# Kernel tuning notes

Measured on AMD Instinct MI355X. Metric: run time of the kernel, lower is better.

Reference implementation:

```python
import jax, jax.numpy as jnp
import numpy as np

B, C, H, W = 32, 512, 32, 32
INNER = C // 8


def setup_inputs() -> dict:
    key = jax.random.key(0)
    k_x, k_f, k_g, k_h = jax.random.split(key, 4)
    x = jax.random.normal(k_x, (B, C, H, W), dtype=jnp.float32)
    # 1x1 Conv1d weights (bias=False) are plain [out, in] matrices.
    s_in = 1.0 / np.sqrt(C)
    Wf = jax.random.uniform(k_f, (INNER, C), dtype=jnp.float32, minval=-s_in, maxval=s_in)
    Wg = jax.random.uniform(k_g, (INNER, C), dtype=jnp.float32, minval=-s_in, maxval=s_in)
    Wh = jax.random.uniform(k_h, (C, C), dtype=jnp.float32, minval=-s_in, maxval=s_in)
    return {"x": x, "Wf": Wf, "Wg": Wg, "Wh": Wh}


def reference(x, Wf, Wg, Wh):
    b, c = x.shape[0], x.shape[1]
    xf = x.reshape(b, c, -1)                       # [B, C, N]
    f = jnp.einsum('ic,bcn->bin', Wf, xf)          # [B, inner, N]
    g = jnp.einsum('ic,bcn->bin', Wg, xf)          # [B, inner, N]
    h = jnp.einsum('oc,bcn->bon', Wh, xf)          # [B, C, N]
    sim = jnp.einsum('bin,bim->bnm', f, g)         # f^T g -> [B, N, N]
    beta = jax.nn.softmax(sim, axis=1)             # softmax over the f-index axis (dim=1)
    o = jnp.einsum('bcn,bnm->bcm', h, beta)        # [B, C, N]
    return o
```

## Files before the change

kernel.cpp:

```cpp
#include <hip/hip_runtime.h>
#include <stdint.h>

#define CDIM 512
#define NPIX 1024
#define IDIM 64

#define WS_BATCH (65536 + 65536 + 524288)
#define XT_OFF   ((size_t)32 * WS_BATCH)
#define XT_ELEMS ((size_t)32 * 1024 * 512)
#define WH_OFF   (XT_OFF + XT_ELEMS)
#define P_OFF    XT_OFF
#define P_ELEMS  ((size_t)32 * 1024 * 1024)
#define LP_OFF   (P_OFF + P_ELEMS)

typedef __bf16 bf16x8 __attribute__((ext_vector_type(8)));
typedef _Float16 f16x8 __attribute__((ext_vector_type(8)));
typedef float f32x4 __attribute__((ext_vector_type(4)));

__device__ __forceinline__ unsigned short f2bf(float f) {
    union { float f; uint32_t u; } v; v.f = f;
    uint32_t u = v.u;
    u += 0x7fffu + ((u >> 16) & 1u);
    return (unsigned short)(u >> 16);
}

__device__ __forceinline__ f32x4 mfma_bf(bf16x8 a, bf16x8 b, f32x4 c) {
    return __builtin_amdgcn_mfma_f32_16x16x32_bf16(a, b, c, 0, 0, 0);
}
__device__ __forceinline__ f32x4 mfma_h(f16x8 a, f16x8 b, f32x4 c) {
    return __builtin_amdgcn_mfma_f32_16x16x32_f16(a, b, c, 0, 0, 0);
}
__device__ __forceinline__ void gld_lds16(const void* g, void* l) {
    __builtin_amdgcn_global_load_lds(
        (const __attribute__((address_space(1))) unsigned int*)g,
        (__attribute__((address_space(3))) unsigned int*)l,
        16, 0, 0);
}
__device__ __forceinline__ void barrier_mem() {
    asm volatile("" ::: "memory");
    __builtin_amdgcn_s_barrier();
    asm volatile("" ::: "memory");
}
__device__ __forceinline__ int swz(int by) { return by ^ (((by >> 7) & 3) << 4); }

__global__ __launch_bounds__(256) void wcvt(
    const float* __restrict__ Wf, const float* __restrict__ Wg,
    const float* __restrict__ Wh, _Float16* __restrict__ wh)
{
    int e = (blockIdx.x * 256 + threadIdx.x) * 4;
    int r = e >> 9, k = e & 511;
    const float* src;
    if (r < 64)       src = Wf + (size_t)r * 512 + k;
    else if (r < 128) src = Wg + (size_t)(r - 64) * 512 + k;
    else              src = Wh + (size_t)(r - 128) * 512 + k;
    float4 v = *(const float4*)src;
    _Float16 h4[4] = {(_Float16)v.x, (_Float16)v.y, (_Float16)v.z, (_Float16)v.w};
    *(ushort4*)(wh + e) = *(ushort4*)h4;
}

__global__ __launch_bounds__(256) void xcvt(
    const float* __restrict__ x, _Float16* __restrict__ xT)
{
    __shared__ _Float16 tile[64][72];
    const int b = blockIdx.z, c0 = blockIdx.y * 64, n0 = blockIdx.x * 64;
    const int t = threadIdx.x;
    const float* xb = x + ((size_t)b * CDIM + c0) * NPIX + n0;
    #pragma unroll
    for (int p = 0; p < 4; ++p) {
        int ci = p * 16 + (t >> 4);
        int nj = (t & 15) * 4;
        float4 v = *(const float4*)(xb + (size_t)ci * NPIX + nj);
        tile[nj + 0][ci] = (_Float16)v.x;
        tile[nj + 1][ci] = (_Float16)v.y;
        tile[nj + 2][ci] = (_Float16)v.z;
        tile[nj + 3][ci] = (_Float16)v.w;
    }
    __syncthreads();
    _Float16* dst = xT + ((size_t)b * NPIX + n0) * CDIM + c0;
    #pragma unroll
    for (int p = 0; p < 2; ++p) {
        int n  = p * 32 + (t >> 3);
        int cc = (t & 7) * 8;
        ushort4 a  = *(ushort4*)&tile[n][cc];
        ushort4 bq = *(ushort4*)&tile[n][cc + 4];
        *(ushort4*)(dst + (size_t)n * CDIM + cc)     = a;
        *(ushort4*)(dst + (size_t)n * CDIM + cc + 4) = bq;
    }
}

__global__ __launch_bounds__(256, 4) void fgh_mfma(
    const _Float16* __restrict__ wh, const _Float16* __restrict__ xT,
    unsigned short* __restrict__ ws)
{
    const int orig = blockIdx.x;
    const int work = (orig & 7) * 160 + (orig >> 3);
    const int b    = work / 40;
    const int tile = work % 40;
    const int tr = tile >> 3, tn = tile & 7;

    const int t = threadIdx.x, lane = t & 63, w = t >> 6;
    const int lr = lane & 15, lg = lane >> 4;
    const int wr = w >> 1, wc = w & 1;

    __shared__ _Float16 Abuf[2][128 * 32];
    __shared__ _Float16 Bbuf[2][128 * 32];

    const _Float16* Ag = wh + (size_t)(tr * 128) * CDIM;
    const _Float16* Bg = xT + ((size_t)b * NPIX + tn * 128) * CDIM;

    int offA[4], offB[4];
    #pragma unroll
    for (int mf = 0; mf < 4; ++mf)
        offA[mf] = swz((wr * 64 + mf * 16 + lr) * 64 + lg * 16);
    #pragma unroll
    for (int nf = 0; nf < 4; ++nf)
        offB[nf] = swz((wc * 64 + nf * 16 + lr) * 64 + lg * 16);

    f32x4 acc[4][4];
    #pragma unroll
    for (int i = 0; i < 4; ++i)
        #pragma unroll
        for (int j = 0; j < 4; ++j) acc[i][j] = (f32x4){0.f, 0.f, 0.f, 0.f};

    auto stage = [&](int buf, int k0) {
        #pragma unroll
        for (int p = 0; p < 2; ++p) {
            int q = p * 256 + t;
            gld_lds16(Ag + (size_t)(q >> 2) * CDIM + k0 + ((q & 3) ^ ((q >> 3) & 3)) * 8,
                      (char*)&Abuf[buf][0] + q * 16);
        }
        #pragma unroll
        for (int p = 0; p < 2; ++p) {
            int q = p * 256 + t;
            gld_lds16(Bg + (size_t)(q >> 2) * CDIM + k0 + ((q & 3) ^ ((q >> 3) & 3)) * 8,
                      (char*)&Bbuf[buf][0] + q * 16);
        }
    };

    stage(0, 0);
    stage(1, 32);

    #pragma unroll 1
    for (int ks = 0; ks < 16; ++ks) {
        const int cur = ks & 1;
        if (ks < 15) asm volatile("s_waitcnt vmcnt(4)" ::: "memory");
        else         asm volatile("s_waitcnt vmcnt(0)" ::: "memory");
        barrier_mem();

        const char* Ab = (const char*)&Abuf[cur][0];
        const char* Bb = (const char*)&Bbuf[cur][0];
        f16x8 af[4];
        #pragma unroll
        for (int mf = 0; mf < 4; ++mf)
            af[mf] = *(const f16x8*)(Ab + offA[mf]);
        #pragma unroll
        for (int nf = 0; nf < 4; ++nf) {
            f16x8 bv = *(const f16x8*)(Bb + offB[nf]);
            #pragma unroll
            for (int mf = 0; mf < 4; ++mf)
                acc[mf][nf] = mfma_h(af[mf], bv, acc[mf][nf]);
        }

        barrier_mem();
        if (ks + 2 < 16) stage(cur, (ks + 2) * 32);
    }

    unsigned short* base = ws + (size_t)b * WS_BATCH;
    const int nbase = tn * 128 + wc * 64;
    if (tr == 0) {
        unsigned short* dst = base + (wr ? 65536 : 0);
        #pragma unroll
        for (int mf = 0; mf < 4; ++mf) {
            const int i0 = mf * 16 + lg * 4;
            #pragma unroll
            for (int nf = 0; nf < 4; ++nf) {
                int n = nbase + nf * 16 + lr;
                ushort4 v;
                v.x = f2bf(acc[mf][nf][0]); v.y = f2bf(acc[mf][nf][1]);
                v.z = f2bf(acc[mf][nf][2]); v.w = f2bf(acc[mf][nf][3]);
                *(ushort4*)(dst + (size_t)n * 64 + i0) = v;
            }
        }
    } else {
        unsigned short* hd = base + 131072;
        const int cbase = (tr - 1) * 128 + wr * 64;
        #pragma unroll
        for (int mf = 0; mf < 4; ++mf)
            #pragma unroll
            for (int nf = 0; nf < 4; ++nf) {
                int n = nbase + nf * 16 + lr;
                #pragma unroll
                for (int j = 0; j < 4; ++j) {
                    int c = cbase + mf * 16 + lg * 4 + j;
                    hd[(size_t)c * NPIX + n] = f2bf(acc[mf][nf][j]);
                }
            }
    }
}

__global__ __launch_bounds__(256, 3) void attn_sm(
    const unsigned short* __restrict__ ws, unsigned short* __restrict__ P,
    float* __restrict__ Lp)
{
    const int orig = blockIdx.x;
    const int work = (orig & 7) * 256 + (orig >> 3);
    const int b    = work >> 6;
    const int tile = work & 63;
    const int mt = tile >> 2, nt = tile & 3;
    const int m0 = mt * 64, n0 = nt * 256;

    const int t = threadIdx.x, lane = t & 63, w = t >> 6;
    const int lr = lane & 15, lg = lane >> 4;

    const unsigned short* fT = ws + (size_t)b * WS_BATCH;
    const unsigned short* gT = fT + 65536;

    __shared__ unsigned short Ab[2][64 * 32];
    __shared__ unsigned short Bb[2][256 * 32];
    __shared__ float red[4][64];
    __shared__ unsigned short rp[4][16][72];

    #pragma unroll
    for (int kc = 0; kc < 2; ++kc) {
        {
            int q = t;
            gld_lds16(gT + (size_t)(m0 + (q >> 2)) * 64 + kc * 32 + ((q & 3) ^ ((q >> 3) & 3)) * 8,
                      (char*)&Ab[kc][0] + q * 16);
        }
        #pragma unroll
        for (int p = 0; p < 4; ++p) {
            int q = p * 256 + t;
            gld_lds16(fT + (size_t)(n0 + (q >> 2)) * 64 + kc * 32 + ((q & 3) ^ ((q >> 3) & 3)) * 8,
                      (char*)&Bb[kc][0] + q * 16);
        }
    }
    __syncthreads();

    int offA[4], offB[4];
    #pragma unroll
    for (int mf = 0; mf < 4; ++mf)
        offA[mf] = swz((mf * 16 + lr) * 64 + lg * 16);
    #pragma unroll
    for (int nf = 0; nf < 4; ++nf)
        offB[nf] = swz((w * 64 + nf * 16 + lr) * 64 + lg * 16);

    f32x4 acc[4][4];
    #pragma unroll
    for (int i = 0; i < 4; ++i)
        #pragma unroll
        for (int j = 0; j < 4; ++j) acc[i][j] = (f32x4){0.f, 0.f, 0.f, 0.f};

    #pragma unroll
    for (int kc = 0; kc < 2; ++kc) {
        const char* Abc = (const char*)&Ab[kc][0];
        const char* Bbc = (const char*)&Bb[kc][0];
        bf16x8 af[4];
        #pragma unroll
        for (int mf = 0; mf < 4; ++mf)
            af[mf] = *(const bf16x8*)(Abc + offA[mf]);
        #pragma unroll
        for (int nf = 0; nf < 4; ++nf) {
            bf16x8 bv = *(const bf16x8*)(Bbc + offB[nf]);
            #pragma unroll
            for (int mf = 0; mf < 4; ++mf)
                acc[mf][nf] = mfma_bf(af[mf], bv, acc[mf][nf]);
        }
    }

    #pragma unroll
    for (int mf = 0; mf < 4; ++mf) {
        #pragma unroll
        for (int j = 0; j < 4; ++j) {
            float s = 0.f;
            #pragma unroll
            for (int nf = 0; nf < 4; ++nf) {
                float e = __expf(acc[mf][nf][j]);
                acc[mf][nf][j] = e;
                s += e;
            }
            s += __shfl_xor(s, 1);
            s += __shfl_xor(s, 2);
            s += __shfl_xor(s, 4);
            s += __shfl_xor(s, 8);
            if (lr == 0) red[w][mf * 16 + lg * 4 + j] = s;
        }
    }
    __syncthreads();
    if (t < 64) {
        float s = red[0][t] + red[1][t] + red[2][t] + red[3][t];
        Lp[(size_t)nt * 32768 + (size_t)b * 1024 + m0 + t] = s;
    }

    unsigned short* Pb = P + (size_t)b * NPIX * NPIX;
    #pragma unroll
    for (int mf = 0; mf < 4; ++mf) {
        #pragma unroll
        for (int nf = 0; nf < 4; ++nf)
            #pragma unroll
            for (int j = 0; j < 4; ++j)
                rp[w][lg * 4 + j][nf * 16 + lr] = f2bf(acc[mf][nf][j]);
        #pragma unroll
        for (int ii = 0; ii < 2; ++ii) {
            int row = ii * 8 + (lane >> 3);
            int ch  = lane & 7;
            ushort4 v0 = *(ushort4*)&rp[w][row][ch * 8];
            ushort4 v1 = *(ushort4*)&rp[w][row][ch * 8 + 4];
            unsigned short* dst = Pb + (size_t)(m0 + mf * 16 + row) * NPIX
                                     + n0 + w * 64 + ch * 8;
            *(ushort4*)(dst)     = v0;
            *(ushort4*)(dst + 4) = v1;
        }
    }
}

__global__ __launch_bounds__(256, 4) void attn_pv(
    const unsigned short* __restrict__ P, const unsigned short* __restrict__ ws,
    const float* __restrict__ Lp, float* __restrict__ out)
{
    const int orig = blockIdx.x;
    const int work = (orig & 7) * 128 + (orig >> 3);
    const int b    = work >> 5;
    const int tile = work & 31;
    const int m0   = (tile >> 2) * 128;
    const int c0   = (tile & 3) * 128;

    const int t = threadIdx.x, lane = t & 63, w = t >> 6;
    const int lr = lane & 15, lg = lane >> 4;
    const int wr = w >> 1, wc = w & 1;

    __shared__ unsigned short Abuf[2][128 * 32];
    __shared__ unsigned short Bbuf[2][128 * 32];

    const unsigned short* Ag = P + ((size_t)b * NPIX + m0) * NPIX;
    const unsigned short* Bg = ws + (size_t)b * WS_BATCH + 131072 + (size_t)c0 * NPIX;

    int offA[4], offB[4];
    #pragma unroll
    for (int mf = 0; mf < 4; ++mf)
        offA[mf] = swz((wr * 64 + mf * 16 + lr) * 64 + lg * 16);
    #pragma unroll
    for (int nf = 0; nf < 4; ++nf)
        offB[nf] = swz((wc * 64 + nf * 16 + lr) * 64 + lg * 16);

    f32x4 acc[4][4];
    #pragma unroll
    for (int i = 0; i < 4; ++i)
        #pragma unroll
        for (int j = 0; j < 4; ++j) acc[i][j] = (f32x4){0.f, 0.f, 0.f, 0.f};

    auto stage = [&](int buf, int k0) {
        #pragma unroll
        for (int p = 0; p < 2; ++p) {
            int q = p * 256 + t;
            gld_lds16(Ag + (size_t)(q >> 2) * NPIX + k0 + ((q & 3) ^ ((q >> 3) & 3)) * 8,
                      (char*)&Abuf[buf][0] + q * 16);
        }
        #pragma unroll
        for (int p = 0; p < 2; ++p) {
            int q = p * 256 + t;
            gld_lds16(Bg + (size_t)(q >> 2) * NPIX + k0 + ((q & 3) ^ ((q >> 3) & 3)) * 8,
                      (char*)&Bbuf[buf][0] + q * 16);
        }
    };

    stage(0, 0);
    stage(1, 32);

    #pragma unroll 1
    for (int ks = 0; ks < 32; ++ks) {
        const int cur = ks & 1;
        if (ks < 31) asm volatile("s_waitcnt vmcnt(4)" ::: "memory");
        else         asm volatile("s_waitcnt vmcnt(0)" ::: "memory");
        barrier_mem();

        const char* Ab = (const char*)&Abuf[cur][0];
        const char* Bb = (const char*)&Bbuf[cur][0];
        bf16x8 af[4];
        #pragma unroll
        for (int mf = 0; mf < 4; ++mf)
            af[mf] = *(const bf16x8*)(Ab + offA[mf]);
        #pragma unroll
        for (int nf = 0; nf < 4; ++nf) {
            bf16x8 bv = *(const bf16x8*)(Bb + offB[nf]);
            #pragma unroll
            for (int mf = 0; mf < 4; ++mf)
                acc[mf][nf] = mfma_bf(af[mf], bv, acc[mf][nf]);
        }

        barrier_mem();
        if (ks + 2 < 32) stage(cur, (ks + 2) * 32);
    }

    #pragma unroll
    for (int mf = 0; mf < 4; ++mf) {
        const size_t mi = (size_t)b * 1024 + m0 + wr * 64 + mf * 16 + lg * 4;
        f32x4 L = *(const f32x4*)&Lp[mi]
                + *(const f32x4*)&Lp[32768 + mi]
                + *(const f32x4*)&Lp[65536 + mi]
                + *(const f32x4*)&Lp[98304 + mi];
        f32x4 rinv;
        #pragma unroll
        for (int j = 0; j < 4; ++j) rinv[j] = 1.0f / L[j];
        #pragma unroll
        for (int nf = 0; nf < 4; ++nf) {
            f32x4 o = acc[mf][nf] * rinv;
            int c = c0 + wc * 64 + nf * 16 + lr;
            int m = m0 + wr * 64 + mf * 16 + lg * 4;
            *(f32x4*)(out + ((size_t)b * CDIM + c) * NPIX + m) = o;
        }
    }
}

extern "C" void kernel_launch(void* const* d_in, const int* in_sizes, int n_in,
                              void* d_out, int out_size, void* d_ws, size_t ws_size,
                              hipStream_t stream) {
    const float* x  = (const float*)d_in[0];
    const float* Wf = (const float*)d_in[1];
    const float* Wg = (const float*)d_in[2];
    const float* Wh = (const float*)d_in[3];
    unsigned short* ws = (unsigned short*)d_ws;
    _Float16* xT = (_Float16*)(ws + XT_OFF);
    _Float16* wh = (_Float16*)(ws + WH_OFF);
    unsigned short* P = ws + P_OFF;
    float* Lp = (float*)(ws + LP_OFF);
    float* out = (float*)d_out;

    wcvt<<<320, 256, 0, stream>>>(Wf, Wg, Wh, wh);
    xcvt<<<dim3(16, 8, 32), 256, 0, stream>>>(x, xT);
    fgh_mfma<<<1280, 256, 0, stream>>>(wh, xT, ws);
    attn_sm<<<2048, 256, 0, stream>>>(ws, P, Lp);
    attn_pv<<<1024, 256, 0, stream>>>(P, ws, Lp, out);
}
```

Before: 132.2 us.

## Enlarge attn_pv tiles to 256x256 with 8 waves and interleaved staged prefetch

Reworks the P·V kernel to compute 256x256 output tiles per 512-thread block with a 64-wide K step, using 128KB of LDS and an XOR-swizzled layout. Global-to-LDS loads are split into halves and interleaved between MFMA groups, and s_setprio is raised around the MFMA bursts. The goal is more reuse per byte loaded and better overlap of loads with math. The trade-off is only 256 blocks on a GPU with many CUs, lower occupancy, and heavy LDS and register use.

```diff
diff --git a/kernel.cpp b/kernel.cpp
--- a/kernel.cpp
+++ b/kernel.cpp
@@ -313,87 +313,112 @@
     }
 }
 
-__global__ __launch_bounds__(256, 4) void attn_pv(
+__global__ __launch_bounds__(512, 2) void attn_pv(
     const unsigned short* __restrict__ P, const unsigned short* __restrict__ ws,
     const float* __restrict__ Lp, float* __restrict__ out)
 {
     const int orig = blockIdx.x;
-    const int work = (orig & 7) * 128 + (orig >> 3);
-    const int b    = work >> 5;
-    const int tile = work & 31;
-    const int m0   = (tile >> 2) * 128;
-    const int c0   = (tile & 3) * 128;
+    const int work = (orig & 7) * 32 + (orig >> 3);
+    const int b    = work >> 3;
+    const int tile = work & 7;
+    const int m0   = (tile >> 1) * 256;
+    const int c0   = (tile & 1) * 256;
 
     const int t = threadIdx.x, lane = t & 63, w = t >> 6;
     const int lr = lane & 15, lg = lane >> 4;
-    const int wr = w >> 1, wc = w & 1;
-
-    __shared__ unsigned short Abuf[2][128 * 32];
-    __shared__ unsigned short Bbuf[2][128 * 32];
+    const int wr = w >> 2, wc = w & 3;
+
+    __shared__ __align__(16) char smem[131072];
 
     const unsigned short* Ag = P + ((size_t)b * NPIX + m0) * NPIX;
     const unsigned short* Bg = ws + (size_t)b * WS_BATCH + 131072 + (size_t)c0 * NPIX;
 
-    int offA[4], offB[4];
-    #pragma unroll
-    for (int mf = 0; mf < 4; ++mf)
-        offA[mf] = swz((wr * 64 + mf * 16 + lr) * 64 + lg * 16);
-    #pragma unroll
-    for (int nf = 0; nf < 4; ++nf)
-        offB[nf] = swz((wc * 64 + nf * 16 + lr) * 64 + lg * 16);
-
-    f32x4 acc[4][4];
-    #pragma unroll
-    for (int i = 0; i < 4; ++i)
+    const int sk0 = ((lg) ^ (lr & 7)) * 16;
+    const int sk1 = ((4 + lg) ^ (lr & 7)) * 16;
+    const int rAbase = (wr * 128 + lr) * 128;
+    const int rBbase = (wc * 64 + lr) * 128;
+
+    f32x4 acc[8][4];
+    #pragma unroll
+    for (int i = 0; i < 8; ++i)
         #pragma unroll
         for (int j = 0; j < 4; ++j) acc[i][j] = (f32x4){0.f, 0.f, 0.f, 0.f};
 
-    auto stage = [&](int buf, int k0) {
-        #pragma unroll
-        for (int p = 0; p < 2; ++p) {
-            int q = p * 256 + t;
-            gld_lds16(Ag + (size_t)(q >> 2) * NPIX + k0 + ((q & 3) ^ ((q >> 3) & 3)) * 8,
-                      (char*)&Abuf[buf][0] + q * 16);
-        }
-        #pragma unroll
-        for (int p = 0; p < 2; ++p) {
-            int q = p * 256 + t;
-            gld_lds16(Bg + (size_t)(q >> 2) * NPIX + k0 + ((q & 3) ^ ((q >> 3) & 3)) * 8,
-                      (char*)&Bbuf[buf][0] + q * 16);
+    auto stage_half = [&](int buf, int isB, int half, int kt) {
+        const unsigned short* G = isB ? Bg : Ag;
+        char* L = smem + isB * 65536 + buf * 32768 + half * 16384;
+        #pragma unroll
+        for (int l = 0; l < 2; ++l) {
+            int q = l * 512 + t;
+            gld_lds16(G + (size_t)(half * 128 + (q >> 3)) * NPIX + kt * 64
+                        + (((q & 7) ^ ((q >> 3) & 7)) * 8),
+                      L + q * 16);
         }
     };
 
-    stage(0, 0);
-    stage(1, 32);
+    stage_half(0, 0, 0, 0); stage_half(0, 0, 1, 0);
+    stage_half(0, 1, 0, 0); stage_half(0, 1, 1, 0);
+    stage_half(1, 1, 0, 1); stage_half(1, 1, 1, 1);
+    asm volatile("s_waitcnt vmcnt(4)" ::: "memory");
+    barrier_mem();
+
+    bf16x8 bfr[4][2];
 
     #pragma unroll 1
-    for (int ks = 0; ks < 32; ++ks) {
-        const int cur = ks & 1;
-        if (ks < 31) asm volatile("s_waitcnt vmcnt(4)" ::: "memory");
-        else         asm volatile("s_waitcnt vmcnt(0)" ::: "memory");
-        barrier_mem();
-
-        const char* Ab = (const char*)&Abuf[cur][0];
-        const char* Bb = (const char*)&Bbuf[cur][0];
-        bf16x8 af[4];
-        #pragma unroll
-        for (int mf = 0; mf < 4; ++mf)
-            af[mf] = *(const bf16x8*)(Ab + offA[mf]);
-        #pragma unroll
-        for (int nf = 0; nf < 4; ++nf) {
-            bf16x8 bv = *(const bf16x8*)(Bb + offB[nf]);
-            #pragma unroll
-            for (int mf = 0; mf < 4; ++mf)
-                acc[mf][nf] = mfma_bf(af[mf], bv, acc[mf][nf]);
-        }
-
-        barrier_mem();
-        if (ks + 2 < 32) stage(cur, (ks + 2) * 32);
-    }
-
-    #pragma unroll
-    for (int mf = 0; mf < 4; ++mf) {
-        const size_t mi = (size_t)b * 1024 + m0 + wr * 64 + mf * 16 + lg * 4;
+    for (int j = 0; j < 8; ++j) {
+        const bool nl = (j < 7);
+        #pragma unroll
+        for (int grp = 0; grp < 2; ++grp) {
+            const char* Abase = smem + grp * 32768;
+            const char* Bbase = smem + 65536 + grp * 32768;
+            #pragma unroll
+            for (int p = 0; p < 4; ++p) {
+                if (p == 0) {
+                    #pragma unroll
+                    for (int nf = 0; nf < 4; ++nf) {
+                        bfr[nf][0] = *(const bf16x8*)(Bbase + rBbase + nf * 2048 + sk0);
+                        bfr[nf][1] = *(const bf16x8*)(Bbase + rBbase + nf * 2048 + sk1);
+                    }
+                }
+                bf16x8 af[2][2];
+                #pragma unroll
+                for (int e = 0; e < 2; ++e) {
+                    af[e][0] = *(const bf16x8*)(Abase + rAbase + (p * 2 + e) * 2048 + sk0);
+                    af[e][1] = *(const bf16x8*)(Abase + rAbase + (p * 2 + e) * 2048 + sk1);
+                }
+                if (grp == 0) {
+                    if (p == 0) stage_half(1, 0, 0, 2 * j + 1);
+                    if (p == 1) stage_half(1, 0, 1, 2 * j + 1);
+                    if (p == 2 && nl) stage_half(0, 1, 0, 2 * j + 2);
+                    if (p == 3 && nl) stage_half(0, 1, 1, 2 * j + 2);
+                } else {
+                    if (p == 0 && nl) stage_half(0, 0, 0, 2 * j + 2);
+                    if (p == 1 && nl) stage_half(0, 0, 1, 2 * j + 2);
+                    if (p == 2 && nl) stage_half(1, 1, 0, 2 * j + 3);
+                    if (p == 3 && nl) stage_half(1, 1, 1, 2 * j + 3);
+                }
+                if (p == 3) {
+                    if (nl) asm volatile("s_waitcnt vmcnt(4)" ::: "memory");
+                    else    asm volatile("s_waitcnt vmcnt(0)" ::: "memory");
+                }
+                barrier_mem();
+                __builtin_amdgcn_s_setprio(1);
+                #pragma unroll
+                for (int ks = 0; ks < 2; ++ks)
+                    #pragma unroll
+                    for (int e = 0; e < 2; ++e)
+                        #pragma unroll
+                        for (int nf = 0; nf < 4; ++nf)
+                            acc[p * 2 + e][nf] =
+                                mfma_bf(af[e][ks], bfr[nf][ks], acc[p * 2 + e][nf]);
+                __builtin_amdgcn_s_setprio(0);
+            }
+        }
+    }
+
+    #pragma unroll
+    for (int mf = 0; mf < 8; ++mf) {
+        const size_t mi = (size_t)b * 1024 + m0 + wr * 128 + mf * 16 + lg * 4;
         f32x4 L = *(const f32x4*)&Lp[mi]
                 + *(const f32x4*)&Lp[32768 + mi]
                 + *(const f32x4*)&Lp[65536 + mi]
@@ -405,7 +430,7 @@
         for (int nf = 0; nf < 4; ++nf) {
             f32x4 o = acc[mf][nf] * rinv;
             int c = c0 + wc * 64 + nf * 16 + lr;
-            int m = m0 + wr * 64 + mf * 16 + lg * 4;
+            int m = m0 + wr * 128 + mf * 16 + lg * 4;
             *(f32x4*)(out + ((size_t)b * CDIM + c) * NPIX + m) = o;
         }
     }
@@ -429,5 +454,5 @@
     xcvt<<<dim3(16, 8, 32), 256, 0, stream>>>(x, xT);
     fgh_mfma<<<1280, 256, 0, stream>>>(wh, xT, ws);
     attn_sm<<<2048, 256, 0, stream>>>(ws, P, Lp);
-    attn_pv<<<1024, 256, 0, stream>>>(P, ws, Lp, out);
-}
+    attn_pv<<<256, 512, 0, stream>>>(P, ws, Lp, out);
+}
```

Result: faster. 119.5 us (-9.6%).
